# Performance work log

Measured on AMD Instinct MI355X. Metric: run time of the kernel, lower is better.

Reference implementation:

```python
import jax, jax.numpy as jnp
import numpy as np

S = 2048      # total tokens
DIM = 1024    # model dim
H = 16        # attention heads
DH = 64       # head dim
BOT = 256     # bottleneck dim
NIMG = 4      # images (equal size)
L = S // NIMG # tokens per image
K = 256       # sparse_k
IH = 4        # indexer heads
ID = 16       # indexer head dim
MAXREL = 64   # hardcoded in module
NBUCK = 2 * MAXREL + 1
GH = IH * 2   # gate MLP hidden (expansion=2)


def setup_inputs() -> dict:
    key = jax.random.key(0)
    ks = jax.random.split(key, 16)
    r = lambda i, sh, s=0.02: jax.random.normal(ks[i], sh, jnp.float32) * s
    return dict(
        hidden_states=jax.random.normal(ks[0], (S, DIM), jnp.float32),
        patch_coords=jax.random.randint(ks[1], (S, 2), 0, 64, dtype=jnp.int32),
        cu_seqlens=jnp.arange(NIMG + 1, dtype=jnp.int32) * L,
        rotary_pos_emb=jax.random.uniform(ks[2], (S, DH // 2), jnp.float32) * 3.0,
        Wq_idx=r(3, (2 * IH * ID, DIM)),
        Wk_idx=r(4, (2 * IH * ID, DIM)),
        W1g=r(5, (GH, IH)), b1g=jnp.zeros((GH,), jnp.float32),
        W2g=r(6, (IH, GH)), b2g=jnp.zeros((IH,), jnp.float32),
        rpe_table=r(7, (NBUCK, IH)),
        Wqkv_d=r(8, (BOT, DIM)), bqkv_d=jnp.zeros((BOT,), jnp.float32),
        Wqkv_u=r(9, (3 * DIM, BOT)), bqkv_u=jnp.zeros((3 * DIM,), jnp.float32),
        Wp_d=r(10, (BOT, DIM)), bp_d=jnp.zeros((BOT,), jnp.float32),
        Wp_u=r(11, (DIM, BOT)), bp_u=jnp.zeros((DIM,), jnp.float32),
        scaler=jnp.ones((1,), jnp.float32),
    )


def _rotate_half(x):
    x1, x2 = jnp.split(x, 2, axis=-1)
    return jnp.concatenate([-x2, x1], axis=-1)


def reference(hidden_states, patch_coords, cu_seqlens, rotary_pos_emb,
              Wq_idx, Wk_idx, W1g, b1g, W2g, b2g, rpe_table,
              Wqkv_d, bqkv_d, Wqkv_u, bqkv_u, Wp_d, bp_d, Wp_u, bp_u, scaler):
    n = cu_seqlens.shape[0] - 1            # images (equal size L)
    Li = hidden_states.shape[0] // n
    neg = jnp.finfo(hidden_states.dtype).min

    # QKV via low-rank bottleneck
    qkv = (hidden_states @ Wqkv_d.T + bqkv_d) @ Wqkv_u.T + bqkv_u  # [S, 3*DIM]
    qkv = qkv.reshape(S, 3, H, DH)
    q, k, v = qkv[:, 0], qkv[:, 1], qkv[:, 2]                      # [S, H, DH]

    # vision RoPE (emb = cat(rpe, rpe))
    emb = jnp.concatenate([rotary_pos_emb, rotary_pos_emb], axis=-1)  # [S, DH]
    cos = jnp.cos(emb)[:, None, :]
    sin = jnpp if False else jnp.sin(emb)[:, None, :]
    q = q * cos + _rotate_half(q) * sin
    k = k * cos + _rotate_half(k) * sin

    # ---- interaction indexer, vmapped over equal-size images ----
    xs = hidden_states.reshape(n, Li, DIM)
    pos = patch_coords[:, 1].reshape(n, Li).astype(jnp.float32)
    qI = (xs @ Wq_idx.T).reshape(n, Li, 2 * IH, ID)
    kI = (xs @ Wk_idx.T).reshape(n, Li, 2 * IH, ID)
    dot = jnp.einsum('nqhd,nkhd->nqkh', qI, kI)                    # [n, L, L, 2*IH]
    data_in, gate_in = dot[..., :IH], dot[..., IH:]
    rel = jnp.clip(pos[:, :, None] - pos[:, None, :], -MAXREL, MAXREL)
    bucket = (rel + MAXREL).astype(jnp.int32)                      # [n, L, L]
    rpe = rpe_table[bucket]                                        # [n, L, L, IH]
    relu_scores = jax.nn.relu(data_in + rpe)
    g = jax.nn.sigmoid(jax.nn.relu((gate_in + rpe) @ W1g.T + b1g) @ W2g.T + b2g)
    index_scores = (relu_scores * g).sum(-1)                       # [n, L, L]

    # top-k sparse mask (0 at selected keys, -inf-ish elsewhere)
    _, topk_idx = jax.lax.top_k(index_scores, K)                   # [n, L, K]
    ni = jnp.arange(n)[:, None, None]
    ri = jnp.arange(Li)[None, :, None]
    mask_local = jnp.full((n, Li, Li), neg, hidden_states.dtype).at[ni, ri, topk_idx].set(0.0)

    # block-diagonal full mask
    mask = jnp.full((S, S), neg, hidden_states.dtype)
    for i in range(n):
        mask = mask.at[i * Li:(i + 1) * Li, i * Li:(i + 1) * Li].set(mask_local[i])

    # dense SDPA with additive mask
    att = jnp.einsum('qhd,khd->hqk', q, k) / jnp.sqrt(jnp.float32(DH)).astype(q.dtype)
    att = att + mask[None]
    p = jax.nn.softmax(att, axis=-1)
    out = jnp.einsum('hqk,khd->qhd', p, v).reshape(S, H * DH)

    final = (out @ Wp_d.T + bp_d) @ Wp_u.T + bp_u
    return final * scaler
```

## Files before the change

kernel.cpp:

```cpp
#include <hip/hip_runtime.h>
#include <hip/hip_bf16.h>

#define S_    2048
#define DIM_  1024
#define H_    16
#define DH_   64
#define BOT_  256
#define NIMG_ 4
#define LI_   512
#define K_    256
#define IH_   4
#define ID_   16
#define MAXREL_ 64
#define NBUCK_ 129
#define GH_   8
#define IDH2_ 128

typedef short bf16x8 __attribute__((ext_vector_type(8)));
typedef float f32x4  __attribute__((ext_vector_type(4)));

__device__ __forceinline__ unsigned short f2bf(float x) {
    unsigned u = __float_as_uint(x);
    return (unsigned short)((u + 0x7fffu + ((u >> 16) & 1u)) >> 16);
}
__device__ __forceinline__ float bf2f(unsigned short h) {
    return __uint_as_float(((unsigned)h) << 16);
}

#define OFF_W1_    2097152
#define OFF_WQ_    2359296
#define OFF_WK_    2490368
#define OFF_WQKVU_ 2621440
#define OFF_WPD_   3407872
#define OFF_WPU_   3670016
#define NSPLIT_    3932160

__global__ __launch_bounds__(256) void split_all_kernel(
    const float* __restrict__ hid, const float* __restrict__ wqd,
    const float* __restrict__ wq,  const float* __restrict__ wk,
    const float* __restrict__ wqu, const float* __restrict__ wpd,
    const float* __restrict__ wpu,
    unsigned short* __restrict__ hi, unsigned short* __restrict__ lo)
{
    long e = ((long)blockIdx.x * 256 + threadIdx.x) * 4;
    if (e >= NSPLIT_) return;
    const float* src; long off;
    if (e < OFF_W1_)         { src = hid; off = 0; }
    else if (e < OFF_WQ_)    { src = wqd; off = OFF_W1_; }
    else if (e < OFF_WK_)    { src = wq;  off = OFF_WQ_; }
    else if (e < OFF_WQKVU_) { src = wk;  off = OFF_WK_; }
    else if (e < OFF_WPD_)   { src = wqu; off = OFF_WQKVU_; }
    else if (e < OFF_WPU_)   { src = wpd; off = OFF_WPD_; }
    else                     { src = wpu; off = OFF_WPU_; }
    float4 v = *(const float4*)(src + (e - off));
    ushort4 h, l;
    h.x = f2bf(v.x); l.x = f2bf(v.x - bf2f(h.x));
    h.y = f2bf(v.y); l.y = f2bf(v.y - bf2f(h.y));
    h.z = f2bf(v.z); l.z = f2bf(v.z - bf2f(h.z));
    h.w = f2bf(v.w); l.w = f2bf(v.w - bf2f(h.w));
    *(ushort4*)&hi[e] = h;
    *(ushort4*)&lo[e] = l;
}

__global__ __launch_bounds__(256) void gemm_bf16x3(
    const unsigned short* __restrict__ Ah, const unsigned short* __restrict__ Al,
    const unsigned short* __restrict__ Bh, const unsigned short* __restrict__ Bl,
    const float* __restrict__ bias, const float* __restrict__ scale_ptr,
    float* __restrict__ Cf, int M, int N, int Kd)
{
    __shared__ unsigned short sAh[128 * 40], sAl[128 * 40];
    __shared__ unsigned short sBh[64 * 40],  sBl[64 * 40];
    int tid = threadIdx.x;
    int lane = tid & 63, wv = tid >> 6;
    int wr = wv >> 1, wc = wv & 1;
    int row0 = blockIdx.y * 128, col0 = blockIdx.x * 64;

    f32x4 acc[4][2];
#pragma unroll
    for (int i = 0; i < 4; i++)
#pragma unroll
        for (int j = 0; j < 2; j++) acc[i][j] = (f32x4){0.f, 0.f, 0.f, 0.f};

    int ar = tid >> 1, ac = (tid & 1) * 16;
    int br = tid >> 2, bc = (tid & 3) * 8;
    const unsigned short* gAh = Ah + (size_t)(row0 + ar) * Kd + ac;
    const unsigned short* gAl = Al + (size_t)(row0 + ar) * Kd + ac;
    const unsigned short* gBh = Bh + (size_t)(col0 + br) * Kd + bc;
    const unsigned short* gBl = Bl + (size_t)(col0 + br) * Kd + bc;
    int am = lane & 15, qk = (lane >> 4) * 8;

    for (int k0 = 0; k0 < Kd; k0 += 32) {
        __syncthreads();
        *(float4*)&sAh[ar * 40 + ac]     = *(const float4*)(gAh + k0);
        *(float4*)&sAh[ar * 40 + ac + 8] = *(const float4*)(gAh + k0 + 8);
        *(float4*)&sAl[ar * 40 + ac]     = *(const float4*)(gAl + k0);
        *(float4*)&sAl[ar * 40 + ac + 8] = *(const float4*)(gAl + k0 + 8);
        *(float4*)&sBh[br * 40 + bc]     = *(const float4*)(gBh + k0);
        *(float4*)&sBl[br * 40 + bc]     = *(const float4*)(gBl + k0);
        __syncthreads();

        bf16x8 ah[4], al[4], bh[2], bl[2];
#pragma unroll
        for (int rt = 0; rt < 4; rt++) {
            int r = wr * 64 + rt * 16 + am;
            ah[rt] = *(const bf16x8*)&sAh[r * 40 + qk];
            al[rt] = *(const bf16x8*)&sAl[r * 40 + qk];
        }
#pragma unroll
        for (int ct = 0; ct < 2; ct++) {
            int c = wc * 32 + ct * 16 + am;
            bh[ct] = *(const bf16x8*)&sBh[c * 40 + qk];
            bl[ct] = *(const bf16x8*)&sBl[c * 40 + qk];
        }
#pragma unroll
        for (int rt = 0; rt < 4; rt++)
#pragma unroll
            for (int ct = 0; ct < 2; ct++) {
                acc[rt][ct] = __builtin_amdgcn_mfma_f32_16x16x32_bf16(ah[rt], bh[ct], acc[rt][ct], 0, 0, 0);
                acc[rt][ct] = __builtin_amdgcn_mfma_f32_16x16x32_bf16(ah[rt], bl[ct], acc[rt][ct], 0, 0, 0);
                acc[rt][ct] = __builtin_amdgcn_mfma_f32_16x16x32_bf16(al[rt], bh[ct], acc[rt][ct], 0, 0, 0);
            }
    }

    float scl = scale_ptr ? *scale_ptr : 1.0f;
    int rq = (lane >> 4) * 4;
#pragma unroll
    for (int rt = 0; rt < 4; rt++)
#pragma unroll
        for (int ct = 0; ct < 2; ct++) {
            int col = col0 + wc * 32 + ct * 16 + am;
            float bz = bias ? bias[col] : 0.0f;
#pragma unroll
            for (int rg = 0; rg < 4; rg++) {
                int row = row0 + wr * 64 + rt * 16 + rq + rg;
                Cf[(size_t)row * N + col] = (acc[rt][ct][rg] + bz) * scl;
            }
        }
}

__global__ __launch_bounds__(256) void gemm_qkv_rope(
    const unsigned short* __restrict__ Ah, const unsigned short* __restrict__ Al,
    const unsigned short* __restrict__ Bh, const unsigned short* __restrict__ Bl,
    const float* __restrict__ bias, const float* __restrict__ rope,
    unsigned short* __restrict__ qkvh, unsigned short* __restrict__ qkvl)
{
    __shared__ unsigned short sAh[128 * 40], sAl[128 * 40];
    __shared__ unsigned short sBh[64 * 40],  sBl[64 * 40];
    int tid = threadIdx.x;
    int lane = tid & 63, wv = tid >> 6;
    int wr = wv >> 1, wc = wv & 1;
    int row0 = blockIdx.y * 128, col0 = blockIdx.x * 64;
    const int Kd = BOT_;

    f32x4 acc[4][2];
#pragma unroll
    for (int i = 0; i < 4; i++)
#pragma unroll
        for (int j = 0; j < 2; j++) acc[i][j] = (f32x4){0.f, 0.f, 0.f, 0.f};

    int ar = tid >> 1, ac = (tid & 1) * 16;
    int br = tid >> 2, bc = (tid & 3) * 8;
    const unsigned short* gAh = Ah + (size_t)(row0 + ar) * Kd + ac;
    const unsigned short* gAl = Al + (size_t)(row0 + ar) * Kd + ac;
    const unsigned short* gBh = Bh + (size_t)(col0 + br) * Kd + bc;
    const unsigned short* gBl = Bl + (size_t)(col0 + br) * Kd + bc;
    int am = lane & 15, qk = (lane >> 4) * 8;

    for (int k0 = 0; k0 < Kd; k0 += 32) {
        __syncthreads();
        *(float4*)&sAh[ar * 40 + ac]     = *(const float4*)(gAh + k0);
        *(float4*)&sAh[ar * 40 + ac + 8] = *(const float4*)(gAh + k0 + 8);
        *(float4*)&sAl[ar * 40 + ac]     = *(const float4*)(gAl + k0);
        *(float4*)&sAl[ar * 40 + ac + 8] = *(const float4*)(gAl + k0 + 8);
        *(float4*)&sBh[br * 40 + bc]     = *(const float4*)(gBh + k0);
        *(float4*)&sBl[br * 40 + bc]     = *(const float4*)(gBl + k0);
        __syncthreads();

        bf16x8 ah[4], al[4], bh[2], bl[2];
#pragma unroll
        for (int rt = 0; rt < 4; rt++) {
            int r = wr * 64 + rt * 16 + am;
            ah[rt] = *(const bf16x8*)&sAh[r * 40 + qk];
            al[rt] = *(const bf16x8*)&sAl[r * 40 + qk];
        }
#pragma unroll
        for (int ct = 0; ct < 2; ct++) {
            int c = ct * 32 + wc * 16 + am;
            bh[ct] = *(const bf16x8*)&sBh[c * 40 + qk];
            bl[ct] = *(const bf16x8*)&sBl[c * 40 + qk];
        }
#pragma unroll
        for (int rt = 0; rt < 4; rt++)
#pragma unroll
            for (int ct = 0; ct < 2; ct++) {
                acc[rt][ct] = __builtin_amdgcn_mfma_f32_16x16x32_bf16(ah[rt], bh[ct], acc[rt][ct], 0, 0, 0);
                acc[rt][ct] = __builtin_amdgcn_mfma_f32_16x16x32_bf16(ah[rt], bl[ct], acc[rt][ct], 0, 0, 0);
                acc[rt][ct] = __builtin_amdgcn_mfma_f32_16x16x32_bf16(al[rt], bh[ct], acc[rt][ct], 0, 0, 0);
            }
    }

    int sec  = blockIdx.x >> 4;
    int hd   = blockIdx.x & 15;
    int d_lo = wc * 16 + am;
    float b1 = bias[col0 + d_lo];
    float b2 = bias[col0 + 32 + d_lo];
    int rq = (lane >> 4) * 4;
#pragma unroll
    for (int rt = 0; rt < 4; rt++)
#pragma unroll
        for (int rg = 0; rg < 4; rg++) {
            int row = row0 + wr * 64 + rt * 16 + rq + rg;
            float x1 = acc[rt][0][rg] + b1;
            float x2 = acc[rt][1][rg] + b2;
            float o1, o2;
            if (sec < 2) {
                float r  = rope[row * 32 + d_lo];
                float cs = cosf(r), sn = sinf(r);
                o1 = x1 * cs - x2 * sn;
                o2 = x2 * cs + x1 * sn;
                if (sec == 0) { o1 *= 0.125f; o2 *= 0.125f; }
            } else {
                o1 = x1; o2 = x2;
            }
            size_t base = (size_t)row * 3072 + sec * 1024 + hd * 64 + d_lo;
            unsigned short h1 = f2bf(o1);
            qkvh[base] = h1;       qkvl[base] = f2bf(o1 - bf2f(h1));
            unsigned short h2 = f2bf(o2);
            qkvh[base + 32] = h2;  qkvl[base + 32] = f2bf(o2 - bf2f(h2));
        }
}

__global__ __launch_bounds__(256) void gemm64_bf16x3(
    const unsigned short* __restrict__ Ah, const unsigned short* __restrict__ Al,
    const unsigned short* __restrict__ Bh, const unsigned short* __restrict__ Bl,
    const float* __restrict__ bias_lo, const float* __restrict__ bias_hi,
    float* __restrict__ Cf, unsigned short* __restrict__ Chi,
    unsigned short* __restrict__ Clo, int M, int N, int Kd, int split_col)
{
    __shared__ unsigned short sAh[64 * 72], sAl[64 * 72];
    __shared__ unsigned short sBh[64 * 72], sBl[64 * 72];
    int tid = threadIdx.x;
    int lane = tid & 63, wv = tid >> 6;
    int wr = wv >> 1, wc = wv & 1;
    int row0 = blockIdx.y * 64, col0 = blockIdx.x * 64;

    f32x4 acc[2][2];
#pragma unroll
    for (int i = 0; i < 2; i++)
#pragma unroll
        for (int j = 0; j < 2; j++) acc[i][j] = (f32x4){0.f, 0.f, 0.f, 0.f};

    int sr = tid >> 2, sc = (tid & 3) * 16;
    const unsigned short* gAh = Ah + (size_t)(row0 + sr) * Kd + sc;
    const unsigned short* gAl = Al + (size_t)(row0 + sr) * Kd + sc;
    const unsigned short* gBh = Bh + (size_t)(col0 + sr) * Kd + sc;
    const unsigned short* gBl = Bl + (size_t)(col0 + sr) * Kd + sc;
    int am = lane & 15, qk = (lane >> 4) * 8;

    for (int k0 = 0; k0 < Kd; k0 += 64) {
        __syncthreads();
        *(float4*)&sAh[sr * 72 + sc]     = *(const float4*)(gAh + k0);
        *(float4*)&sAh[sr * 72 + sc + 8] = *(const float4*)(gAh + k0 + 8);
        *(float4*)&sAl[sr * 72 + sc]     = *(const float4*)(gAl + k0);
        *(float4*)&sAl[sr * 72 + sc + 8] = *(const float4*)(gAl + k0 + 8);
        *(float4*)&sBh[sr * 72 + sc]     = *(const float4*)(gBh + k0);
        *(float4*)&sBh[sr * 72 + sc + 8] = *(const float4*)(gBh + k0 + 8);
        *(float4*)&sBl[sr * 72 + sc]     = *(const float4*)(gBl + k0);
        *(float4*)&sBl[sr * 72 + sc + 8] = *(const float4*)(gBl + k0 + 8);
        __syncthreads();

#pragma unroll
        for (int ks = 0; ks < 2; ks++) {
            bf16x8 ah[2], al[2], bh[2], bl[2];
#pragma unroll
            for (int rt = 0; rt < 2; rt++) {
                int r = wr * 32 + rt * 16 + am;
                ah[rt] = *(const bf16x8*)&sAh[r * 72 + ks * 32 + qk];
                al[rt] = *(const bf16x8*)&sAl[r * 72 + ks * 32 + qk];
            }
#pragma unroll
            for (int ct = 0; ct < 2; ct++) {
                int c = wc * 32 + ct * 16 + am;
                bh[ct] = *(const bf16x8*)&sBh[c * 72 + ks * 32 + qk];
                bl[ct] = *(const bf16x8*)&sBl[c * 72 + ks * 32 + qk];
            }
#pragma unroll
            for (int rt = 0; rt < 2; rt++)
#pragma unroll
                for (int ct = 0; ct < 2; ct++) {
                    acc[rt][ct] = __builtin_amdgcn_mfma_f32_16x16x32_bf16(ah[rt], bh[ct], acc[rt][ct], 0, 0, 0);
                    acc[rt][ct] = __builtin_amdgcn_mfma_f32_16x16x32_bf16(ah[rt], bl[ct], acc[rt][ct], 0, 0, 0);
                    acc[rt][ct] = __builtin_amdgcn_mfma_f32_16x16x32_bf16(al[rt], bh[ct], acc[rt][ct], 0, 0, 0);
                }
        }
    }

    int rq = (lane >> 4) * 4;
#pragma unroll
    for (int rt = 0; rt < 2; rt++)
#pragma unroll
        for (int ct = 0; ct < 2; ct++) {
            int col = col0 + wc * 32 + ct * 16 + am;
#pragma unroll
            for (int rg = 0; rg < 4; rg++) {
                int row = row0 + wr * 32 + rt * 16 + rq + rg;
                float v = acc[rt][ct][rg];
                if (col < split_col) {
                    if (bias_lo) v += bias_lo[col];
                    size_t idx = (size_t)row * split_col + col;
                    unsigned short hh = f2bf(v);
                    Chi[idx] = hh;
                    Clo[idx] = f2bf(v - bf2f(hh));
                } else {
                    if (bias_hi) v += bias_hi[col - split_col];
                    Cf[(size_t)row * (N - split_col) + col - split_col] = v;
                }
            }
        }
}

__global__ __launch_bounds__(256) void score_topk_kernel(
    const float* __restrict__ qIk,
    const int* __restrict__ coords, const float* __restrict__ rpe_table,
    const float* __restrict__ W1g, const float* __restrict__ b1g,
    const float* __restrict__ W2g, const float* __restrict__ b2g,
    unsigned* __restrict__ selmask)
{
    __shared__ float skI[64][132];
    __shared__ float sqI2[4][IDH2_];
    __shared__ unsigned skeys[4][LI_];
    __shared__ int shist[4][256];
    __shared__ float srpe[NBUCK_ * IH_];
    __shared__ float sW1[GH_ * IH_], sb1[GH_], sW2[IH_ * GH_], sb2[IH_];

    int tid  = threadIdx.x;
    int lane = tid & 63;
    int wv   = tid >> 6;
    int row  = blockIdx.x * 4 + wv;
    int n    = (blockIdx.x * 4) >> 9;

    for (int i = tid; i < NBUCK_ * IH_; i += 256) srpe[i] = rpe_table[i];
    if (tid < 32) sW1[tid] = W1g[tid];
    else if (tid < 64) sW2[tid - 32] = W2g[tid - 32];
    else if (tid < 72) sb1[tid - 64] = b1g[tid - 64];
    else if (tid < 76) sb2[tid - 72] = b2g[tid - 72];
    for (int i = tid; i < 4 * IDH2_; i += 256)
        sqI2[i >> 7][i & 127] =
            qIk[(size_t)(blockIdx.x * 4 + (i >> 7)) * 256 + (i & 127)];
    int pq = coords[row * 2 + 1];

    for (int kt = 0; kt < 8; kt++) {
        __syncthreads();
        {
            int r  = tid >> 2;
            int d0 = (tid & 3) * 32;
            const float* src = qIk + (size_t)(n * LI_ + kt * 64 + r) * 256 + 128 + d0;
#pragma unroll
            for (int j = 0; j < 8; j++)
                *(float4*)&skI[r][d0 + j * 4] = *(const float4*)(src + j * 4);
        }
        __syncthreads();

        int kloc = lane;
        int kg   = kt * 64 + kloc;
        const float* sq = &sqI2[wv][0];
        float dh[8];
#pragma unroll
        for (int hh = 0; hh < 8; hh++) {
            float acc = 0.0f;
#pragma unroll
            for (int d = 0; d < 16; d += 4) {
                float4 kv = *(const float4*)&skI[kloc][hh * 16 + d];
                acc += sq[hh * 16 + d + 0] * kv.x + sq[hh * 16 + d + 1] * kv.y +
                       sq[hh * 16 + d + 2] * kv.z + sq[hh * 16 + d + 3] * kv.w;
            }
            dh[hh] = acc;
        }
        int pk = coords[(n * LI_ + kg) * 2 + 1];
        int rel = pq - pk;
        rel = rel < -MAXREL_ ? -MAXREL_ : (rel > MAXREL_ ? MAXREL_ : rel);
        const float* rp = srpe + (rel + MAXREL_) * IH_;
        float t1[GH_];
#pragma unroll
        for (int g = 0; g < GH_; g++) t1[g] = sb1[g];
#pragma unroll
        for (int j = 0; j < IH_; j++) {
            float gate = dh[IH_ + j] + rp[j];
#pragma unroll
            for (int g = 0; g < GH_; g++) t1[g] += gate * sW1[g * IH_ + j];
        }
#pragma unroll
        for (int g = 0; g < GH_; g++) t1[g] = fmaxf(t1[g], 0.0f);
        float score = 0.0f;
#pragma unroll
        for (int j = 0; j < IH_; j++) {
            float t2 = sb2[j];
#pragma unroll
            for (int g = 0; g < GH_; g++) t2 += t1[g] * sW2[j * GH_ + g];
            float sg = 1.0f / (1.0f + expf(-t2));
            float rs = fmaxf(dh[j] + rp[j], 0.0f);
            score += rs * sg;
        }
        unsigned bits = __float_as_uint(score);
        skeys[wv][kg] = (bits & 0x80000000u) ? ~bits : (bits | 0x80000000u);
    }

    unsigned pref = 0u;
    int kcur = K_;
    const unsigned himask[4] = {0u, 0xFF000000u, 0xFFFF0000u, 0xFFFFFF00u};
#pragma unroll
    for (int pass = 0; pass < 4; pass++) {
        int shift = 24 - pass * 8;
        unsigned hm = himask[pass];
        *(int4*)&shist[wv][4 * lane] = make_int4(0, 0, 0, 0);
#pragma unroll
        for (int c = 0; c < 8; c++) {
            unsigned key = skeys[wv][c * 64 + lane];
            if ((key & hm) == pref) atomicAdd(&shist[wv][(key >> shift) & 255], 1);
        }
        int4 b4 = *(const int4*)&shist[wv][4 * lane];
        int b[4] = {b4.x, b4.y, b4.z, b4.w};
        int t = b[0] + b[1] + b[2] + b[3];
        int Ssum = t;
#pragma unroll
        for (int off = 1; off < 64; off <<= 1) {
            int u = __shfl_down(Ssum, off, 64);
            if (lane + off < 64) Ssum += u;
        }
        int E = Ssum - t;
        int cs[5];
        cs[4] = E;
        cs[3] = b[3] + E;
        cs[2] = b[2] + cs[3];
        cs[1] = b[1] + cs[2];
        cs[0] = b[0] + cs[1];
        bool found = false;
        unsigned cpref = 0u; int ck = 0;
#pragma unroll
        for (int j = 0; j < 4; j++) {
            if (!found && cs[j] >= kcur && cs[j + 1] < kcur) {
                found = true;
                cpref = pref | ((unsigned)(4 * lane + j) << shift);
                ck = kcur - cs[j + 1];
            }
        }
        unsigned long long bm = __ballot(found);
        int src = __ffsll((long long)bm) - 1;
        pref = (unsigned)__shfl((int)cpref, src, 64);
        kcur = __shfl(ck, src, 64);
    }
    unsigned Tu = pref;

    unsigned long long bg[8], be[8];
#pragma unroll
    for (int c = 0; c < 8; c++) {
        unsigned key = skeys[wv][c * 64 + lane];
        bg[c] = __ballot(key > Tu);
        be[c] = __ballot(key == Tu);
    }
    if (lane < 16) {
        int total_gt = 0;
#pragma unroll
        for (int c = 0; c < 8; c++) total_gt += __popcll(bg[c]);
        int base = 0;
#pragma unroll
        for (int c = 0; c < 8; c++) {
            if (2 * c < lane)     base += __popc((unsigned)be[c]);
            if (2 * c + 1 < lane) base += __popc((unsigned)(be[c] >> 32));
        }
        unsigned gw = (unsigned)(bg[lane >> 1] >> (32 * (lane & 1)));
        unsigned ew = (unsigned)(be[lane >> 1] >> (32 * (lane & 1)));
        int ne = K_ - total_gt - base;
        int pc = __popc(ew);
        int m = ne < 0 ? 0 : (ne > pc ? pc : ne);
        while (pc > m) { ew ^= (1u << (31 - __clz(ew))); pc--; }
        selmask[(size_t)row * 16 + lane] = gw | ew;
    }
}

__global__ __launch_bounds__(256) void attn_kernel(
    const unsigned short* __restrict__ qkvh, const unsigned short* __restrict__ qkvl,
    const unsigned* __restrict__ selmask,
    unsigned short* __restrict__ outh, unsigned short* __restrict__ outl)
{
    __shared__ unsigned short Qh[64 * 72],  Ql[64 * 72];
    __shared__ unsigned short Kh[64 * 72],  Kl[64 * 72];
    __shared__ unsigned short VTh[64 * 72], VTl[64 * 72];
    __shared__ unsigned short Ph[64 * 72],  Pl[64 * 72];
    __shared__ unsigned Ms[64][16];

    int b  = blockIdx.x;
    int qt = b >> 6;
    int nh = b & 63;
    int h  = nh & 15;
    int n  = nh >> 4;
    int tid = threadIdx.x;
    int lane = tid & 63, w = tid >> 6;
    int lane15 = lane & 15, quad = lane >> 4;
    int q0 = n * LI_ + qt * 64;

    for (int i = tid; i < 64 * 16; i += 256)
        Ms[i >> 4][i & 15] = selmask[(size_t)(q0 + (i >> 4)) * 16 + (i & 15)];

    {
        int r = tid >> 2, c0 = (tid & 3) * 16;
        size_t off = (size_t)(q0 + r) * 3072 + h * 64 + c0;
        *(uint4*)&Qh[r * 72 + c0]     = *(const uint4*)(qkvh + off);
        *(uint4*)&Qh[r * 72 + c0 + 8] = *(const uint4*)(qkvh + off + 8);
        *(uint4*)&Ql[r * 72 + c0]     = *(const uint4*)(qkvl + off);
        *(uint4*)&Ql[r * 72 + c0 + 8] = *(const uint4*)(qkvl + off + 8);
    }
    __syncthreads();
    bf16x8 qfh[2], qfl[2];
#pragma unroll
    for (int ks = 0; ks < 2; ks++) {
        qfh[ks] = *(const bf16x8*)&Qh[(16 * w + lane15) * 72 + ks * 32 + quad * 8];
        qfl[ks] = *(const bf16x8*)&Ql[(16 * w + lane15) * 72 + ks * 32 + quad * 8];
    }

    int kr = tid >> 2, kc0 = (tid & 3) * 16;
    int vd = lane, vk0 = w * 16;
    const size_t kbase = (size_t)n * LI_ * 3072 + 1024 + h * 64;
    const size_t vbase = (size_t)n * LI_ * 3072 + 2048 + h * 64;

    uint4 pkh0, pkh1, pkl0, pkl1;
    unsigned short pvh[16], pvl[16];

#define LOADT(KT)                                                              \
    {                                                                          \
        size_t offK = kbase + (size_t)((KT) * 64 + kr) * 3072 + kc0;           \
        pkh0 = *(const uint4*)(qkvh + offK);                                   \
        pkh1 = *(const uint4*)(qkvh + offK + 8);                               \
        pkl0 = *(const uint4*)(qkvl + offK);                                   \
        pkl1 = *(const uint4*)(qkvl + offK + 8);                               \
        size_t offV = vbase + (size_t)((KT) * 64 + vk0) * 3072 + vd;           \
        _Pragma("unroll")                                                      \
        for (int j = 0; j < 16; j++) {                                         \
            pvh[j] = qkvh[offV + (size_t)j * 3072];                            \
            pvl[j] = qkvl[offV + (size_t)j * 3072];                            \
        }                                                                      \
    }

    LOADT(0);

    f32x4 o_acc[4];
#pragma unroll
    for (int i = 0; i < 4; i++) o_acc[i] = (f32x4){0.f, 0.f, 0.f, 0.f};
    float rsum[4] = {};

    for (int kt = 0; kt < 8; kt++) {
        __syncthreads();
        *(uint4*)&Kh[kr * 72 + kc0]      = pkh0;
        *(uint4*)&Kh[kr * 72 + kc0 + 8]  = pkh1;
        *(uint4*)&Kl[kr * 72 + kc0]      = pkl0;
        *(uint4*)&Kl[kr * 72 + kc0 + 8]  = pkl1;
        *(uint4*)&VTh[vd * 72 + vk0]     = *(uint4*)&pvh[0];
        *(uint4*)&VTh[vd * 72 + vk0 + 8] = *(uint4*)&pvh[8];
        *(uint4*)&VTl[vd * 72 + vk0]     = *(uint4*)&pvl[0];
        *(uint4*)&VTl[vd * 72 + vk0 + 8] = *(uint4*)&pvl[8];
        __syncthreads();

        if (kt < 7) LOADT(kt + 1);

        f32x4 s_acc[4];
#pragma unroll
        for (int nt = 0; nt < 4; nt++) s_acc[nt] = (f32x4){0.f, 0.f, 0.f, 0.f};
        __builtin_amdgcn_s_setprio(1);
#pragma unroll
        for (int nt = 0; nt < 4; nt++) {
#pragma unroll
            for (int ks = 0; ks < 2; ks++) {
                bf16x8 kfh = *(const bf16x8*)&Kh[(16 * nt + lane15) * 72 + ks * 32 + quad * 8];
                bf16x8 kfl = *(const bf16x8*)&Kl[(16 * nt + lane15) * 72 + ks * 32 + quad * 8];
                s_acc[nt] = __builtin_amdgcn_mfma_f32_16x16x32_bf16(qfh[ks], kfh, s_acc[nt], 0, 0, 0);
                s_acc[nt] = __builtin_amdgcn_mfma_f32_16x16x32_bf16(qfh[ks], kfl, s_acc[nt], 0, 0, 0);
                s_acc[nt] = __builtin_amdgcn_mfma_f32_16x16x32_bf16(qfl[ks], kfh, s_acc[nt], 0, 0, 0);
            }
        }
        __builtin_amdgcn_s_setprio(0);

#pragma unroll
        for (int nt = 0; nt < 4; nt++) {
            int kb = kt * 64 + nt * 16 + lane15;
            int wi = kb >> 5, bit = kb & 31;
#pragma unroll
            for (int reg = 0; reg < 4; reg++) {
                int qloc = 16 * w + quad * 4 + reg;
                unsigned mw = Ms[qloc][wi];
                float p = ((mw >> bit) & 1u) ? __expf(s_acc[nt][reg]) : 0.0f;
                rsum[reg] += p;
                unsigned short ph = f2bf(p);
                Ph[qloc * 72 + nt * 16 + lane15] = ph;
                Pl[qloc * 72 + nt * 16 + lane15] = f2bf(p - bf2f(ph));
            }
        }

        {
            bf16x8 pfh[2], pfl[2];
#pragma unroll
            for (int ks = 0; ks < 2; ks++) {
                pfh[ks] = *(const bf16x8*)&Ph[(16 * w + lane15) * 72 + ks * 32 + quad * 8];
                pfl[ks] = *(const bf16x8*)&Pl[(16 * w + lane15) * 72 + ks * 32 + quad * 8];
            }
            __builtin_amdgcn_s_setprio(1);
#pragma unroll
            for (int dt = 0; dt < 4; dt++) {
#pragma unroll
                for (int ks = 0; ks < 2; ks++) {
                    bf16x8 vfh = *(const bf16x8*)&VTh[(16 * dt + lane15) * 72 + ks * 32 + quad * 8];
                    bf16x8 vfl = *(const bf16x8*)&VTl[(16 * dt + lane15) * 72 + ks * 32 + quad * 8];
                    o_acc[dt] = __builtin_amdgcn_mfma_f32_16x16x32_bf16(pfh[ks], vfh, o_acc[dt], 0, 0, 0);
                    o_acc[dt] = __builtin_amdgcn_mfma_f32_16x16x32_bf16(pfh[ks], vfl, o_acc[dt], 0, 0, 0);
                    o_acc[dt] = __builtin_amdgcn_mfma_f32_16x16x32_bf16(pfl[ks], vfh, o_acc[dt], 0, 0, 0);
                }
            }
            __builtin_amdgcn_s_setprio(0);
        }
    }
#undef LOADT

#pragma unroll
    for (int reg = 0; reg < 4; reg++) {
        rsum[reg] += __shfl_xor(rsum[reg], 1, 64);
        rsum[reg] += __shfl_xor(rsum[reg], 2, 64);
        rsum[reg] += __shfl_xor(rsum[reg], 4, 64);
        rsum[reg] += __shfl_xor(rsum[reg], 8, 64);
    }

#pragma unroll
    for (int dt = 0; dt < 4; dt++) {
#pragma unroll
        for (int reg = 0; reg < 4; reg++) {
            float v = o_acc[dt][reg] / rsum[reg];
            size_t ob = (size_t)(q0 + 16 * w + quad * 4 + reg) * 1024 + h * 64 + 16 * dt + lane15;
            unsigned short hh = f2bf(v);
            outh[ob] = hh;
            outl[ob] = f2bf(v - bf2f(hh));
        }
    }
}

extern "C" void kernel_launch(void* const* d_in, const int* in_sizes, int n_in,
                              void* d_out, int out_size, void* d_ws, size_t ws_size,
                              hipStream_t stream)
{
    const float* hidden  = (const float*)d_in[0];
    const int*   coords  = (const int*)d_in[1];
    const float* rope    = (const float*)d_in[3];
    const float* Wq_idx  = (const float*)d_in[4];
    const float* Wk_idx  = (const float*)d_in[5];
    const float* W1g     = (const float*)d_in[6];
    const float* b1g     = (const float*)d_in[7];
    const float* W2g     = (const float*)d_in[8];
    const float* b2g     = (const float*)d_in[9];
    const float* rpe     = (const float*)d_in[10];
    const float* Wqkv_d  = (const float*)d_in[11];
    const float* bqkv_d  = (const float*)d_in[12];
    const float* Wqkv_u  = (const float*)d_in[13];
    const float* bqkv_u  = (const float*)d_in[14];
    const float* Wp_d    = (const float*)d_in[15];
    const float* bp_d    = (const float*)d_in[16];
    const float* Wp_u    = (const float*)d_in[17];
    const float* bp_u    = (const float*)d_in[18];
    const float* scaler  = (const float*)d_in[19];
    float* out = (float*)d_out;

    unsigned short* sp_hi  = (unsigned short*)d_ws;
    unsigned short* sp_lo  = sp_hi + NSPLIT_;
    unsigned short* mid_hi = sp_lo + NSPLIT_;
    unsigned short* mid_lo = mid_hi + (size_t)S_ * BOT_;
    float* qkv = (float*)(mid_lo + (size_t)S_ * BOT_);
    float* qIk = qkv + (size_t)S_ * 3 * DIM_;
    unsigned* selmask = (unsigned*)(qIk + (size_t)S_ * 256);
    unsigned short* qkvh = (unsigned short*)(selmask + (size_t)S_ * 16);
    unsigned short* qkvl = qkvh + (size_t)S_ * 3 * DIM_;

    split_all_kernel<<<(NSPLIT_ / 4 + 255) / 256, 256, 0, stream>>>(
        hidden, Wqkv_d, Wq_idx, Wk_idx, Wqkv_u, Wp_d, Wp_u, sp_hi, sp_lo);

    gemm64_bf16x3<<<dim3(512 / 64, S_ / 64), 256, 0, stream>>>(
        sp_hi, sp_lo, sp_hi + OFF_W1_, sp_lo + OFF_W1_,
        bqkv_d, nullptr, qIk, mid_hi, mid_lo, S_, 512, DIM_, 256);

    score_topk_kernel<<<S_ / 4, 256, 0, stream>>>(
        qIk, coords, rpe, W1g, b1g, W2g, b2g, selmask);

    gemm_qkv_rope<<<dim3(3 * DIM_ / 64, S_ / 128), 256, 0, stream>>>(
        mid_hi, mid_lo, sp_hi + OFF_WQKVU_, sp_lo + OFF_WQKVU_,
        bqkv_u, rope, qkvh, qkvl);

    attn_kernel<<<NIMG_ * H_ * 8, 256, 0, stream>>>(qkvh, qkvl, selmask, sp_hi, sp_lo);

    gemm64_bf16x3<<<dim3(BOT_ / 64, S_ / 64), 256, 0, stream>>>(
        sp_hi, sp_lo, sp_hi + OFF_WPD_, sp_lo + OFF_WPD_,
        bp_d, nullptr, nullptr, mid_hi, mid_lo, S_, BOT_, DIM_, BOT_);

    gemm_bf16x3<<<dim3(DIM_ / 64, S_ / 128), 256, 0, stream>>>(
        mid_hi, mid_lo, sp_hi + OFF_WPU_, sp_lo + OFF_WPU_,
        bp_u, scaler, out, S_, DIM_, BOT_);
}
```

Measured before the change: 245.6 us.

## Merge score/top-k and QKV-up GEMM into one launch; precompute RoPE trig

Combines the independent indexer score/top-k kernel and the QKV up-projection GEMM with RoPE into one heterogeneous launch, where blocks below 512 run scoring and the rest run GEMM tiles, so the two can overlap on the GPU and one launch is saved. RoPE cos/sin values are now computed once in the split kernel and read from a table, instead of being recomputed with cosf/sinf in each GEMM epilogue. In exchange, both halves share one static shared-memory allocation sized for the larger scoring layout, which may lower GEMM-block occupancy, and the trig tables add an extra buffer that is written and then read.

```diff
diff --git a/kernel.cpp b/kernel.cpp
--- a/kernel.cpp
+++ b/kernel.cpp
@@ -34,16 +34,30 @@
 #define OFF_WPD_   3407872
 #define OFF_WPU_   3670016
 #define NSPLIT_    3932160
+#define NTRIG_     65536
 
 __global__ __launch_bounds__(256) void split_all_kernel(
     const float* __restrict__ hid, const float* __restrict__ wqd,
     const float* __restrict__ wq,  const float* __restrict__ wk,
     const float* __restrict__ wqu, const float* __restrict__ wpd,
-    const float* __restrict__ wpu,
-    unsigned short* __restrict__ hi, unsigned short* __restrict__ lo)
+    const float* __restrict__ wpu, const float* __restrict__ rope,
+    unsigned short* __restrict__ hi, unsigned short* __restrict__ lo,
+    float* __restrict__ cost, float* __restrict__ sint)
 {
     long e = ((long)blockIdx.x * 256 + threadIdx.x) * 4;
-    if (e >= NSPLIT_) return;
+    if (e >= NSPLIT_ + NTRIG_) return;
+    if (e >= NSPLIT_) {
+        long t = e - NSPLIT_;
+        float4 r = *(const float4*)(rope + t);
+        float4 c, s;
+        c.x = cosf(r.x); s.x = sinf(r.x);
+        c.y = cosf(r.y); s.y = sinf(r.y);
+        c.z = cosf(r.z); s.z = sinf(r.z);
+        c.w = cosf(r.w); s.w = sinf(r.w);
+        *(float4*)&cost[t] = c;
+        *(float4*)&sint[t] = s;
+        return;
+    }
     const float* src; long off;
     if (e < OFF_W1_)         { src = hid; off = 0; }
     else if (e < OFF_WQ_)    { src = wqd; off = OFF_W1_; }
@@ -138,98 +152,6 @@
         }
 }
 
-__global__ __launch_bounds__(256) void gemm_qkv_rope(
-    const unsigned short* __restrict__ Ah, const unsigned short* __restrict__ Al,
-    const unsigned short* __restrict__ Bh, const unsigned short* __restrict__ Bl,
-    const float* __restrict__ bias, const float* __restrict__ rope,
-    unsigned short* __restrict__ qkvh, unsigned short* __restrict__ qkvl)
-{
-    __shared__ unsigned short sAh[128 * 40], sAl[128 * 40];
-    __shared__ unsigned short sBh[64 * 40],  sBl[64 * 40];
-    int tid = threadIdx.x;
-    int lane = tid & 63, wv = tid >> 6;
-    int wr = wv >> 1, wc = wv & 1;
-    int row0 = blockIdx.y * 128, col0 = blockIdx.x * 64;
-    const int Kd = BOT_;
-
-    f32x4 acc[4][2];
-#pragma unroll
-    for (int i = 0; i < 4; i++)
-#pragma unroll
-        for (int j = 0; j < 2; j++) acc[i][j] = (f32x4){0.f, 0.f, 0.f, 0.f};
-
-    int ar = tid >> 1, ac = (tid & 1) * 16;
-    int br = tid >> 2, bc = (tid & 3) * 8;
-    const unsigned short* gAh = Ah + (size_t)(row0 + ar) * Kd + ac;
-    const unsigned short* gAl = Al + (size_t)(row0 + ar) * Kd + ac;
-    const unsigned short* gBh = Bh + (size_t)(col0 + br) * Kd + bc;
-    const unsigned short* gBl = Bl + (size_t)(col0 + br) * Kd + bc;
-    int am = lane & 15, qk = (lane >> 4) * 8;
-
-    for (int k0 = 0; k0 < Kd; k0 += 32) {
-        __syncthreads();
-        *(float4*)&sAh[ar * 40 + ac]     = *(const float4*)(gAh + k0);
-        *(float4*)&sAh[ar * 40 + ac + 8] = *(const float4*)(gAh + k0 + 8);
-        *(float4*)&sAl[ar * 40 + ac]     = *(const float4*)(gAl + k0);
-        *(float4*)&sAl[ar * 40 + ac + 8] = *(const float4*)(gAl + k0 + 8);
-        *(float4*)&sBh[br * 40 + bc]     = *(const float4*)(gBh + k0);
-        *(float4*)&sBl[br * 40 + bc]     = *(const float4*)(gBl + k0);
-        __syncthreads();
-
-        bf16x8 ah[4], al[4], bh[2], bl[2];
-#pragma unroll
-        for (int rt = 0; rt < 4; rt++) {
-            int r = wr * 64 + rt * 16 + am;
-            ah[rt] = *(const bf16x8*)&sAh[r * 40 + qk];
-            al[rt] = *(const bf16x8*)&sAl[r * 40 + qk];
-        }
-#pragma unroll
-        for (int ct = 0; ct < 2; ct++) {
-            int c = ct * 32 + wc * 16 + am;
-            bh[ct] = *(const bf16x8*)&sBh[c * 40 + qk];
-            bl[ct] = *(const bf16x8*)&sBl[c * 40 + qk];
-        }
-#pragma unroll
-        for (int rt = 0; rt < 4; rt++)
-#pragma unroll
-            for (int ct = 0; ct < 2; ct++) {
-                acc[rt][ct] = __builtin_amdgcn_mfma_f32_16x16x32_bf16(ah[rt], bh[ct], acc[rt][ct], 0, 0, 0);
-                acc[rt][ct] = __builtin_amdgcn_mfma_f32_16x16x32_bf16(ah[rt], bl[ct], acc[rt][ct], 0, 0, 0);
-                acc[rt][ct] = __builtin_amdgcn_mfma_f32_16x16x32_bf16(al[rt], bh[ct], acc[rt][ct], 0, 0, 0);
-            }
-    }
-
-    int sec  = blockIdx.x >> 4;
-    int hd   = blockIdx.x & 15;
-    int d_lo = wc * 16 + am;
-    float b1 = bias[col0 + d_lo];
-    float b2 = bias[col0 + 32 + d_lo];
-    int rq = (lane >> 4) * 4;
-#pragma unroll
-    for (int rt = 0; rt < 4; rt++)
-#pragma unroll
-        for (int rg = 0; rg < 4; rg++) {
-            int row = row0 + wr * 64 + rt * 16 + rq + rg;
-            float x1 = acc[rt][0][rg] + b1;
-            float x2 = acc[rt][1][rg] + b2;
-            float o1, o2;
-            if (sec < 2) {
-                float r  = rope[row * 32 + d_lo];
-                float cs = cosf(r), sn = sinf(r);
-                o1 = x1 * cs - x2 * sn;
-                o2 = x2 * cs + x1 * sn;
-                if (sec == 0) { o1 *= 0.125f; o2 *= 0.125f; }
-            } else {
-                o1 = x1; o2 = x2;
-            }
-            size_t base = (size_t)row * 3072 + sec * 1024 + hd * 64 + d_lo;
-            unsigned short h1 = f2bf(o1);
-            qkvh[base] = h1;       qkvl[base] = f2bf(o1 - bf2f(h1));
-            unsigned short h2 = f2bf(o2);
-            qkvh[base + 32] = h2;  qkvl[base + 32] = f2bf(o2 - bf2f(h2));
-        }
-}
-
 __global__ __launch_bounds__(256) void gemm64_bf16x3(
     const unsigned short* __restrict__ Ah, const unsigned short* __restrict__ Al,
     const unsigned short* __restrict__ Bh, const unsigned short* __restrict__ Bl,
@@ -319,19 +241,25 @@
         }
 }
 
-__global__ __launch_bounds__(256) void score_topk_kernel(
+#define SCORE_BLOCKS_ 512
+
+__device__ __forceinline__ void score_body(
+    char* smem,
     const float* __restrict__ qIk,
     const int* __restrict__ coords, const float* __restrict__ rpe_table,
     const float* __restrict__ W1g, const float* __restrict__ b1g,
     const float* __restrict__ W2g, const float* __restrict__ b2g,
     unsigned* __restrict__ selmask)
 {
-    __shared__ float skI[64][132];
-    __shared__ float sqI2[4][IDH2_];
-    __shared__ unsigned skeys[4][LI_];
-    __shared__ int shist[4][256];
-    __shared__ float srpe[NBUCK_ * IH_];
-    __shared__ float sW1[GH_ * IH_], sb1[GH_], sW2[IH_ * GH_], sb2[IH_];
+    float    (*skI)[132]  = (float(*)[132])smem;
+    float    (*sqI2)[128] = (float(*)[128])(smem + 33792);
+    unsigned (*skeys)[512]= (unsigned(*)[512])(smem + 35840);
+    int      (*shist)[256]= (int(*)[256])(smem + 44032);
+    float*   srpe = (float*)(smem + 48128);
+    float*   sW1  = (float*)(smem + 50192);
+    float*   sb1  = (float*)(smem + 50320);
+    float*   sW2  = (float*)(smem + 50352);
+    float*   sb2  = (float*)(smem + 50480);
 
     int tid  = threadIdx.x;
     int lane = tid & 63;
@@ -475,6 +403,125 @@
         int m = ne < 0 ? 0 : (ne > pc ? pc : ne);
         while (pc > m) { ew ^= (1u << (31 - __clz(ew))); pc--; }
         selmask[(size_t)row * 16 + lane] = gw | ew;
+    }
+}
+
+__device__ __forceinline__ void gemm_qkv_body(
+    char* smem, int gb,
+    const unsigned short* __restrict__ Ah, const unsigned short* __restrict__ Al,
+    const unsigned short* __restrict__ Bh, const unsigned short* __restrict__ Bl,
+    const float* __restrict__ bias, const float* __restrict__ cost,
+    const float* __restrict__ sint,
+    unsigned short* __restrict__ qkvh, unsigned short* __restrict__ qkvl)
+{
+    unsigned short* sAh = (unsigned short*)smem;
+    unsigned short* sAl = sAh + 128 * 40;
+    unsigned short* sBh = sAl + 128 * 40;
+    unsigned short* sBl = sBh + 64 * 40;
+
+    int bx = gb % 48, by = gb / 48;
+    int tid = threadIdx.x;
+    int lane = tid & 63, wv = tid >> 6;
+    int wr = wv >> 1, wc = wv & 1;
+    int row0 = by * 128, col0 = bx * 64;
+    const int Kd = BOT_;
+
+    f32x4 acc[4][2];
+#pragma unroll
+    for (int i = 0; i < 4; i++)
+#pragma unroll
+        for (int j = 0; j < 2; j++) acc[i][j] = (f32x4){0.f, 0.f, 0.f, 0.f};
+
+    int ar = tid >> 1, ac = (tid & 1) * 16;
+    int br = tid >> 2, bc = (tid & 3) * 8;
+    const unsigned short* gAh = Ah + (size_t)(row0 + ar) * Kd + ac;
+    const unsigned short* gAl = Al + (size_t)(row0 + ar) * Kd + ac;
+    const unsigned short* gBh = Bh + (size_t)(col0 + br) * Kd + bc;
+    const unsigned short* gBl = Bl + (size_t)(col0 + br) * Kd + bc;
+    int am = lane & 15, qk = (lane >> 4) * 8;
+
+    for (int k0 = 0; k0 < Kd; k0 += 32) {
+        __syncthreads();
+        *(float4*)&sAh[ar * 40 + ac]     = *(const float4*)(gAh + k0);
+        *(float4*)&sAh[ar * 40 + ac + 8] = *(const float4*)(gAh + k0 + 8);
+        *(float4*)&sAl[ar * 40 + ac]     = *(const float4*)(gAl + k0);
+        *(float4*)&sAl[ar * 40 + ac + 8] = *(const float4*)(gAl + k0 + 8);
+        *(float4*)&sBh[br * 40 + bc]     = *(const float4*)(gBh + k0);
+        *(float4*)&sBl[br * 40 + bc]     = *(const float4*)(gBl + k0);
+        __syncthreads();
+
+        bf16x8 ah[4], al[4], bh[2], bl[2];
+#pragma unroll
+        for (int rt = 0; rt < 4; rt++) {
+            int r = wr * 64 + rt * 16 + am;
+            ah[rt] = *(const bf16x8*)&sAh[r * 40 + qk];
+            al[rt] = *(const bf16x8*)&sAl[r * 40 + qk];
+        }
+#pragma unroll
+        for (int ct = 0; ct < 2; ct++) {
+            int c = ct * 32 + wc * 16 + am;
+            bh[ct] = *(const bf16x8*)&sBh[c * 40 + qk];
+            bl[ct] = *(const bf16x8*)&sBl[c * 40 + qk];
+        }
+#pragma unroll
+        for (int rt = 0; rt < 4; rt++)
+#pragma unroll
+            for (int ct = 0; ct < 2; ct++) {
+                acc[rt][ct] = __builtin_amdgcn_mfma_f32_16x16x32_bf16(ah[rt], bh[ct], acc[rt][ct], 0, 0, 0);
+                acc[rt][ct] = __builtin_amdgcn_mfma_f32_16x16x32_bf16(ah[rt], bl[ct], acc[rt][ct], 0, 0, 0);
+                acc[rt][ct] = __builtin_amdgcn_mfma_f32_16x16x32_bf16(al[rt], bh[ct], acc[rt][ct], 0, 0, 0);
+            }
+    }
+
+    int sec  = bx >> 4;
+    int hd   = bx & 15;
+    int d_lo = wc * 16 + am;
+    float b1 = bias[col0 + d_lo];
+    float b2 = bias[col0 + 32 + d_lo];
+    int rq = (lane >> 4) * 4;
+#pragma unroll
+    for (int rt = 0; rt < 4; rt++)
+#pragma unroll
+        for (int rg = 0; rg < 4; rg++) {
+            int row = row0 + wr * 64 + rt * 16 + rq + rg;
+            float x1 = acc[rt][0][rg] + b1;
+            float x2 = acc[rt][1][rg] + b2;
+            float o1, o2;
+            if (sec < 2) {
+                float cs = cost[row * 32 + d_lo];
+                float sn = sint[row * 32 + d_lo];
+                o1 = x1 * cs - x2 * sn;
+                o2 = x2 * cs + x1 * sn;
+                if (sec == 0) { o1 *= 0.125f; o2 *= 0.125f; }
+            } else {
+                o1 = x1; o2 = x2;
+            }
+            size_t base = (size_t)row * 3072 + sec * 1024 + hd * 64 + d_lo;
+            unsigned short h1 = f2bf(o1);
+            qkvh[base] = h1;       qkvl[base] = f2bf(o1 - bf2f(h1));
+            unsigned short h2 = f2bf(o2);
+            qkvh[base + 32] = h2;  qkvl[base + 32] = f2bf(o2 - bf2f(h2));
+        }
+}
+
+__global__ __launch_bounds__(256) void score_qkv_fused(
+    const float* __restrict__ qIk,
+    const int* __restrict__ coords, const float* __restrict__ rpe_table,
+    const float* __restrict__ W1g, const float* __restrict__ b1g,
+    const float* __restrict__ W2g, const float* __restrict__ b2g,
+    unsigned* __restrict__ selmask,
+    const unsigned short* __restrict__ Ah, const unsigned short* __restrict__ Al,
+    const unsigned short* __restrict__ Bh, const unsigned short* __restrict__ Bl,
+    const float* __restrict__ bias, const float* __restrict__ cost,
+    const float* __restrict__ sint,
+    unsigned short* __restrict__ qkvh, unsigned short* __restrict__ qkvl)
+{
+    __shared__ __align__(16) char smem[50688];
+    if (blockIdx.x < SCORE_BLOCKS_) {
+        score_body(smem, qIk, coords, rpe_table, W1g, b1g, W2g, b2g, selmask);
+    } else {
+        gemm_qkv_body(smem, blockIdx.x - SCORE_BLOCKS_,
+                      Ah, Al, Bh, Bl, bias, cost, sint, qkvh, qkvl);
     }
 }
 
@@ -674,20 +721,21 @@
     unsigned* selmask = (unsigned*)(qIk + (size_t)S_ * 256);
     unsigned short* qkvh = (unsigned short*)(selmask + (size_t)S_ * 16);
     unsigned short* qkvl = qkvh + (size_t)S_ * 3 * DIM_;
-
-    split_all_kernel<<<(NSPLIT_ / 4 + 255) / 256, 256, 0, stream>>>(
-        hidden, Wqkv_d, Wq_idx, Wk_idx, Wqkv_u, Wp_d, Wp_u, sp_hi, sp_lo);
+    float* cost = (float*)(qkvl + (size_t)S_ * 3 * DIM_);
+    float* sint = cost + NTRIG_;
+
+    split_all_kernel<<<((NSPLIT_ + NTRIG_) / 4 + 255) / 256, 256, 0, stream>>>(
+        hidden, Wqkv_d, Wq_idx, Wk_idx, Wqkv_u, Wp_d, Wp_u, rope,
+        sp_hi, sp_lo, cost, sint);
 
     gemm64_bf16x3<<<dim3(512 / 64, S_ / 64), 256, 0, stream>>>(
         sp_hi, sp_lo, sp_hi + OFF_W1_, sp_lo + OFF_W1_,
         bqkv_d, nullptr, qIk, mid_hi, mid_lo, S_, 512, DIM_, 256);
 
-    score_topk_kernel<<<S_ / 4, 256, 0, stream>>>(
-        qIk, coords, rpe, W1g, b1g, W2g, b2g, selmask);
-
-    gemm_qkv_rope<<<dim3(3 * DIM_ / 64, S_ / 128), 256, 0, stream>>>(
+    score_qkv_fused<<<SCORE_BLOCKS_ + 768, 256, 0, stream>>>(
+        qIk, coords, rpe, W1g, b1g, W2g, b2g, selmask,
         mid_hi, mid_lo, sp_hi + OFF_WQKVU_, sp_lo + OFF_WQKVU_,
-        bqkv_u, rope, qkvh, qkvl);
+        bqkv_u, cost, sint, qkvh, qkvl);
 
     attn_kernel<<<NIMG_ * H_ * 8, 256, 0, stream>>>(qkvh, qkvl, selmask, sp_hi, sp_lo);
 
```

Measured after the change: 263.0 us. 7.1% more time.
